# Optimization experiments

Measured on AMD Instinct MI355X. Metric: run time of the kernel, lower is better.

Reference implementation:

```python
import jax, jax.numpy as jnp
import numpy as np

HIDDEN = 1024
B, S = 4, 2048

def setup_inputs() -> dict:
    key = jax.random.key(0)
    k1, k2 = jax.random.split(key)
    qkv = jax.random.normal(k1, (B, S, HIDDEN), dtype=jnp.float32)
    mask = jnp.ones((B, S), dtype=jnp.float32)
    W_qkv = jax.random.normal(k2, (HIDDEN, 3 * HIDDEN), dtype=jnp.float32) * (HIDDEN ** -0.5)
    b_qkv = jnp.zeros((3 * HIDDEN,), dtype=jnp.float32)
    return {"qkv": qkv, "mask": mask, "W_qkv": W_qkv, "b_qkv": b_qkv}

def reference(qkv, mask, W_qkv, b_qkv):
    scale = HIDDEN ** -0.5
    proj = jnp.einsum("bsi,ih->bsh", qkv, W_qkv) + b_qkv  # [B,S,3H]
    q, k, v = jnp.split(proj, 3, axis=-1)                  # each [B,S,H]
    q = q * scale
    scores = jnp.einsum("bqh,bkh->bqk", q, k)              # [B,S,S]
    scores = scores + (1.0 - mask)[:, None, :] * -10000.0
    dist = jax.nn.softmax(scores, axis=-1)                 # dropout = identity (eval)
    return jnp.einsum("bqk,bkh->bqh", dist, v)             # [B,S,H]
```

## Files before the change

### kernel.cpp

```cpp
#include <hip/hip_runtime.h>
#include <hip/hip_bf16.h>

#define HID   1024
#define H3    3072
#define SEQ   2048
#define NB    4
#define MTOT  8192

typedef __bf16 bf16;
typedef bf16  bf16x4 __attribute__((ext_vector_type(4)));
typedef bf16  bf16x8 __attribute__((ext_vector_type(8)));
typedef float f32x4  __attribute__((ext_vector_type(4)));

#define MFMA16(a, b, c) __builtin_amdgcn_mfma_f32_16x16x32_bf16((a), (b), (c), 0, 0, 0)

#define GLOAD_LDS16(gp, lp)                                                     \
    __builtin_amdgcn_global_load_lds(                                           \
        (const __attribute__((address_space(1))) void*)(gp),                    \
        (__attribute__((address_space(3))) void*)(lp), 16, 0, 0)

#define FENCE() asm volatile("" ::: "memory")

__device__ __forceinline__ void stage_half(
    const bf16* __restrict__ G, long ld, long row0, long col0,
    char* dstbase, int w, int lane)
{
    const int r  = lane >> 2;
    const int c0 = ((lane & 3) * 8) ^ (((lane >> 5) & 1) << 4);
#pragma unroll
    for (int l = 0; l < 2; ++l) {
        const int sh = l * 8 + w;
        const bf16* src = G + (row0 + (long)((sh >> 1) * 16 + r)) * ld
                            + col0 + ((sh & 1) * 32 + c0);
        GLOAD_LDS16(src, dstbase + sh * 1024);
    }
}

__device__ __forceinline__ void gemm256_core(
    const bf16* __restrict__ A, long lda,
    const bf16* __restrict__ Bt, long ldb,
    long m0, long n0, int NT, char* lds, f32x4 (&acc)[8][4])
{
    const int tid = threadIdx.x, lane = tid & 63, w = tid >> 6;
    const int lr = lane & 15, lkg = lane >> 4;
    const int subA = (w >> 2) * 8;
    const int subB = (w & 3) * 4;
    const int inner = lr * 64 + (((lkg * 8) ^ ((lr >> 3) << 4)) << 1);

    char* A0b = lds;
    char* B0b = lds + 32768;
    char* A1b = lds + 65536;
    char* B1b = lds + 98304;

    stage_half(A,  lda, m0,        0, A0b,          w, lane);
    stage_half(A,  lda, m0 + 128,  0, A0b + 16384,  w, lane);
    stage_half(Bt, ldb, n0,        0, B0b,          w, lane);
    stage_half(Bt, ldb, n0 + 128,  0, B0b + 16384,  w, lane);
    stage_half(Bt, ldb, n0,       64, B1b,          w, lane);
    stage_half(Bt, ldb, n0 + 128, 64, B1b + 16384,  w, lane);
    asm volatile("s_waitcnt vmcnt(0)" ::: "memory");
    __builtin_amdgcn_s_barrier();
    FENCE();

    bf16x8 aR[4][2], bR[4][2];

    for (int t = 0; t < NT; ++t) {
        char* Ac = (t & 1) ? A1b : A0b;
        char* Bc = (t & 1) ? B1b : B0b;
        char* An = (t & 1) ? A0b : A1b;
        const long kA = (long)(t + 1) * 64;
        const long kB = (long)(t + 2) * 64;
        const bool doA = (t + 1 < NT), doB = (t + 2 < NT);

#pragma unroll
        for (int mf = 0; mf < 4; ++mf)
#pragma unroll
            for (int ks = 0; ks < 2; ++ks)
                aR[mf][ks] = *(const bf16x8*)(Ac + ((subA + mf) * 2 + ks) * 1024 + inner);
#pragma unroll
        for (int nf = 0; nf < 2; ++nf)
#pragma unroll
            for (int ks = 0; ks < 2; ++ks)
                bR[nf][ks] = *(const bf16x8*)(Bc + ((subB + nf) * 2 + ks) * 1024 + inner);
        if (doA) stage_half(A, lda, m0, kA, An, w, lane);
        __builtin_amdgcn_s_barrier();
        __builtin_amdgcn_s_setprio(1);
#pragma unroll
        for (int mf = 0; mf < 4; ++mf)
#pragma unroll
            for (int nf = 0; nf < 2; ++nf)
#pragma unroll
                for (int ks = 0; ks < 2; ++ks)
                    acc[mf][nf] = MFMA16(aR[mf][ks], bR[nf][ks], acc[mf][nf]);
        __builtin_amdgcn_s_setprio(0);
        __builtin_amdgcn_s_barrier();
        FENCE();

#pragma unroll
        for (int nf = 0; nf < 2; ++nf)
#pragma unroll
            for (int ks = 0; ks < 2; ++ks)
                bR[2 + nf][ks] = *(const bf16x8*)(Bc + ((subB + 2 + nf) * 2 + ks) * 1024 + inner);
        if (doA) stage_half(A, lda, m0 + 128, kA, An + 16384, w, lane);
        __builtin_amdgcn_s_barrier();
        __builtin_amdgcn_s_setprio(1);
#pragma unroll
        for (int mf = 0; mf < 4; ++mf)
#pragma unroll
            for (int nf = 0; nf < 2; ++nf)
#pragma unroll
                for (int ks = 0; ks < 2; ++ks)
                    acc[mf][2 + nf] = MFMA16(aR[mf][ks], bR[2 + nf][ks], acc[mf][2 + nf]);
        __builtin_amdgcn_s_setprio(0);
        __builtin_amdgcn_s_barrier();
        FENCE();

#pragma unroll
        for (int mf = 0; mf < 4; ++mf)
#pragma unroll
            for (int ks = 0; ks < 2; ++ks)
                aR[mf][ks] = *(const bf16x8*)(Ac + ((subA + 4 + mf) * 2 + ks) * 1024 + inner);
        if (doB) stage_half(Bt, ldb, n0, kB, Bc, w, lane);
        __builtin_amdgcn_s_barrier();
        __builtin_amdgcn_s_setprio(1);
#pragma unroll
        for (int mf = 0; mf < 4; ++mf)
#pragma unroll
            for (int nf = 0; nf < 2; ++nf)
#pragma unroll
                for (int ks = 0; ks < 2; ++ks)
                    acc[4 + mf][nf] = MFMA16(aR[mf][ks], bR[nf][ks], acc[4 + mf][nf]);
        __builtin_amdgcn_s_setprio(0);
        __builtin_amdgcn_s_barrier();
        FENCE();

        if (doB) {
            stage_half(Bt, ldb, n0 + 128, kB, Bc + 16384, w, lane);
            asm volatile("s_waitcnt vmcnt(4)" ::: "memory");
        } else {
            asm volatile("s_waitcnt vmcnt(0)" ::: "memory");
        }
        __builtin_amdgcn_s_barrier();
        __builtin_amdgcn_s_setprio(1);
#pragma unroll
        for (int mf = 0; mf < 4; ++mf)
#pragma unroll
            for (int nf = 0; nf < 2; ++nf)
#pragma unroll
                for (int ks = 0; ks < 2; ++ks)
                    acc[4 + mf][2 + nf] = MFMA16(aR[mf][ks], bR[2 + nf][ks], acc[4 + mf][2 + nf]);
        __builtin_amdgcn_s_setprio(0);
        __builtin_amdgcn_s_barrier();
        FENCE();
    }
}

__device__ __forceinline__ void gemm_h_core(
    const bf16* __restrict__ A, long lda,
    const bf16* __restrict__ Bt, long ldb,
    long m0, long n0, int NT, char* lds, f32x4 (&acc)[4][4])
{
    const int tid = threadIdx.x, lane = tid & 63, w = tid >> 6;
    const int lr = lane & 15, lkg = lane >> 4;
    const int subA = (w >> 2) * 4;
    const int subB = (w & 3) * 4;
    const int inner = lr * 64 + (((lkg * 8) ^ ((lr >> 3) << 4)) << 1);

    char* A0b = lds;
    char* B0b = lds + 16384;
    char* A1b = lds + 49152;
    char* B1b = lds + 65536;

    stage_half(A,  lda, m0,        0, A0b,          w, lane);
    stage_half(Bt, ldb, n0,        0, B0b,          w, lane);
    stage_half(Bt, ldb, n0 + 128,  0, B0b + 16384,  w, lane);
    stage_half(Bt, ldb, n0,       64, B1b,          w, lane);
    stage_half(Bt, ldb, n0 + 128, 64, B1b + 16384,  w, lane);
    asm volatile("s_waitcnt vmcnt(0)" ::: "memory");
    __builtin_amdgcn_s_barrier();
    FENCE();

    bf16x8 aR[2][2], bR[4][2];

    for (int t = 0; t < NT; ++t) {
        char* Ac = (t & 1) ? A1b : A0b;
        char* Bc = (t & 1) ? B1b : B0b;
        char* An = (t & 1) ? A0b : A1b;
        const long kA = (long)(t + 1) * 64;
        const long kB = (long)(t + 2) * 64;
        const bool doA = (t + 1 < NT), doB = (t + 2 < NT);

#pragma unroll
        for (int mf = 0; mf < 2; ++mf)
#pragma unroll
            for (int ks = 0; ks < 2; ++ks)
                aR[mf][ks] = *(const bf16x8*)(Ac + ((subA + mf) * 2 + ks) * 1024 + inner);
#pragma unroll
        for (int nf = 0; nf < 2; ++nf)
#pragma unroll
            for (int ks = 0; ks < 2; ++ks)
                bR[nf][ks] = *(const bf16x8*)(Bc + ((subB + nf) * 2 + ks) * 1024 + inner);
        if (doA) stage_half(A, lda, m0, kA, An, w, lane);
        __builtin_amdgcn_s_barrier();
        __builtin_amdgcn_s_setprio(1);
#pragma unroll
        for (int mf = 0; mf < 2; ++mf)
#pragma unroll
            for (int nf = 0; nf < 2; ++nf)
#pragma unroll
                for (int ks = 0; ks < 2; ++ks)
                    acc[mf][nf] = MFMA16(aR[mf][ks], bR[nf][ks], acc[mf][nf]);
        __builtin_amdgcn_s_setprio(0);
        __builtin_amdgcn_s_barrier();
        FENCE();

#pragma unroll
        for (int nf = 0; nf < 2; ++nf)
#pragma unroll
            for (int ks = 0; ks < 2; ++ks)
                bR[2 + nf][ks] = *(const bf16x8*)(Bc + ((subB + 2 + nf) * 2 + ks) * 1024 + inner);
        __builtin_amdgcn_s_barrier();
        __builtin_amdgcn_s_setprio(1);
#pragma unroll
        for (int mf = 0; mf < 2; ++mf)
#pragma unroll
            for (int nf = 0; nf < 2; ++nf)
#pragma unroll
                for (int ks = 0; ks < 2; ++ks)
                    acc[mf][2 + nf] = MFMA16(aR[mf][ks], bR[2 + nf][ks], acc[mf][2 + nf]);
        __builtin_amdgcn_s_setprio(0);
        __builtin_amdgcn_s_barrier();
        FENCE();

#pragma unroll
        for (int mf = 0; mf < 2; ++mf)
#pragma unroll
            for (int ks = 0; ks < 2; ++ks)
                aR[mf][ks] = *(const bf16x8*)(Ac + ((subA + 2 + mf) * 2 + ks) * 1024 + inner);
        if (doB) {
            stage_half(Bt, ldb, n0,       kB, Bc,         w, lane);
            stage_half(Bt, ldb, n0 + 128, kB, Bc + 16384, w, lane);
        }
        __builtin_amdgcn_s_barrier();
        __builtin_amdgcn_s_setprio(1);
#pragma unroll
        for (int mf = 0; mf < 2; ++mf)
#pragma unroll
            for (int nf = 0; nf < 2; ++nf)
#pragma unroll
                for (int ks = 0; ks < 2; ++ks)
                    acc[2 + mf][nf] = MFMA16(aR[mf][ks], bR[nf][ks], acc[2 + mf][nf]);
        __builtin_amdgcn_s_setprio(0);
        __builtin_amdgcn_s_barrier();
        FENCE();

        if (doB) {
            asm volatile("s_waitcnt vmcnt(4)" ::: "memory");
        } else {
            asm volatile("s_waitcnt vmcnt(0)" ::: "memory");
        }
        __builtin_amdgcn_s_barrier();
        __builtin_amdgcn_s_setprio(1);
#pragma unroll
        for (int mf = 0; mf < 2; ++mf)
#pragma unroll
            for (int nf = 0; nf < 2; ++nf)
#pragma unroll
                for (int ks = 0; ks < 2; ++ks)
                    acc[2 + mf][2 + nf] = MFMA16(aR[mf][ks], bR[2 + nf][ks], acc[2 + mf][2 + nf]);
        __builtin_amdgcn_s_setprio(0);
        __builtin_amdgcn_s_barrier();
        FENCE();
    }
}

__global__ __launch_bounds__(256) void conv_kernel(
    const float* __restrict__ X, const float* __restrict__ W,
    bf16* __restrict__ Xb, bf16* __restrict__ Wt, float* __restrict__ lbuf)
{
    __shared__ bf16 T[64][66];
    const int bid = blockIdx.x;
    if (bid < 4096) {
        const long i = ((long)bid * 256 + threadIdx.x) * 8;
        float4 a = *(const float4*)(X + i);
        float4 b = *(const float4*)(X + i + 4);
        bf16x8 o;
        o[0] = (bf16)a.x; o[1] = (bf16)a.y; o[2] = (bf16)a.z; o[3] = (bf16)a.w;
        o[4] = (bf16)b.x; o[5] = (bf16)b.y; o[6] = (bf16)b.z; o[7] = (bf16)b.w;
        *(bf16x8*)(Xb + i) = o;
    } else if (bid < 4096 + 768) {
        const int b2 = bid - 4096;
        const int n0 = (b2 % 48) * 64, k0 = (b2 / 48) * 64;
        const int r = threadIdx.x >> 2, s = threadIdx.x & 3;
        const float* wp = W + (size_t)(k0 + r) * H3 + n0 + s * 16;
#pragma unroll
        for (int q = 0; q < 4; ++q) {
            float4 a = *(const float4*)(wp + q * 4);
            T[r][s * 16 + q * 4 + 0] = (bf16)a.x;
            T[r][s * 16 + q * 4 + 1] = (bf16)a.y;
            T[r][s * 16 + q * 4 + 2] = (bf16)a.z;
            T[r][s * 16 + q * 4 + 3] = (bf16)a.w;
        }
        __syncthreads();
        bf16x8 o0, o1;
#pragma unroll
        for (int i = 0; i < 8; ++i) o0[i] = T[s * 16 + i][r];
#pragma unroll
        for (int i = 0; i < 8; ++i) o1[i] = T[s * 16 + 8 + i][r];
        bf16* op = Wt + (size_t)(n0 + r) * HID + k0 + s * 16;
        *(bf16x8*)op       = o0;
        *(bf16x8*)(op + 8) = o1;
    } else {
        for (int i = threadIdx.x; i < MTOT; i += 256) lbuf[i] = 0.0f;
    }
}

__global__ __launch_bounds__(512, 2) void proj_h(
    const bf16* __restrict__ Xb, const bf16* __restrict__ Wt,
    const float* __restrict__ bias,
    bf16* __restrict__ Qb, bf16* __restrict__ Kb, bf16* __restrict__ Vt)
{
    __shared__ __attribute__((aligned(16))) char lds[98304];
    const int x = blockIdx.x & 7, q = blockIdx.x >> 3;
    const int bm = x * 8 + (q & 7);
    const int bn = q >> 3;

    f32x4 acc[4][4] = {};
    gemm_h_core(Xb, HID, Wt, HID, (long)bm * 128, (long)bn * 256, 16, lds, acc);

    const int tid = threadIdx.x, lane = tid & 63, w = tid >> 6;
    const int lr = lane & 15, lkg = lane >> 4;
    const int wmL = (w >> 2) * 64;
    const int wnL = (w & 3) * 64;
    const int seg = bn >> 2;

    __syncthreads();
    bf16* sm_ = (bf16*)lds;

    if (seg < 2) {
        const float qs = (seg == 0) ? 0.03125f : 1.0f;
#pragma unroll
        for (int nf = 0; nf < 4; ++nf) {
            const int nl = wnL + nf * 16 + lr;
            const float bv = bias[bn * 256 + nl];
#pragma unroll
            for (int mf = 0; mf < 4; ++mf) {
                const int ml = wmL + mf * 16 + lkg * 4;
#pragma unroll
                for (int j = 0; j < 4; ++j)
                    sm_[(ml + j) * 264 + nl] = (bf16)((acc[mf][nf][j] + bv) * qs);
            }
        }
        __syncthreads();
        bf16* dst = (seg == 0) ? Qb : Kb;
        const long rowbase = (long)bm * 128;
        const long colbase = (long)(bn & 3) * 256;
#pragma unroll
        for (int it = 0; it < 8; ++it) {
            const int ml = (tid >> 5) + it * 16;
            const int nc = (tid & 31) * 8;
            bf16x8 vv = *(const bf16x8*)&sm_[ml * 264 + nc];
            *(bf16x8*)&dst[(rowbase + ml) * HID + colbase + nc] = vv;
        }
    } else {
#pragma unroll
        for (int nf = 0; nf < 4; ++nf) {
            const int nl = wnL + nf * 16 + lr;
            const float bv = bias[bn * 256 + nl];
#pragma unroll
            for (int mf = 0; mf < 4; ++mf) {
                const int ml = wmL + mf * 16 + lkg * 4;
                bf16x4 pk;
#pragma unroll
                for (int j = 0; j < 4; ++j) pk[j] = (bf16)(acc[mf][nf][j] + bv);
                *(bf16x4*)&sm_[nl * 136 + ml] = pk;
            }
        }
        __syncthreads();
        const int  bb = bm >> 4;
        const long s0 = (long)(bm & 15) * 128;
        const long h0 = (long)(bn - 8) * 256;
#pragma unroll
        for (int it = 0; it < 8; ++it) {
            const int nl = (tid >> 4) + it * 32;
            const int mc = (tid & 15) * 8;
            bf16x8 vv = *(const bf16x8*)&sm_[nl * 136 + mc];
            *(bf16x8*)&Vt[((long)(bb << 10) + h0 + nl) * SEQ + s0 + mc] = vv;
        }
    }
}

__global__ __launch_bounds__(512, 2) void qk_gemm2(
    const bf16* __restrict__ Qb, const bf16* __restrict__ Kb,
    bf16* __restrict__ Pb, float* __restrict__ lbuf,
    const float* __restrict__ mask, int b_base)
{
    __shared__ __attribute__((aligned(16))) char lds[135168];
    __shared__ float lsum[2][128][4];
    const int z = blockIdx.z, b = b_base + z;

    f32x4 acc[8][4] = {};
    gemm256_core(Qb + (size_t)b * SEQ * HID, HID,
                 Kb + (size_t)b * SEQ * HID, HID,
                 (long)blockIdx.x * 256, (long)blockIdx.y * 256, 16, lds, acc);

    const int tid = threadIdx.x, lane = tid & 63, w = tid >> 6;
    const int lr = lane & 15, lkg = lane >> 4;
    const int mh = w >> 2;
    const int nw = w & 3;

    __syncthreads();
    bf16* smP = (bf16*)lds;

    float mterm[4];
#pragma unroll
    for (int nf = 0; nf < 4; ++nf) {
        const int col = (int)blockIdx.y * 256 + nw * 64 + nf * 16 + lr;
        mterm[nf] = (1.0f - mask[(size_t)b * SEQ + col]) * -10000.0f;
    }

#pragma unroll
    for (int mf = 0; mf < 8; ++mf) {
#pragma unroll
        for (int j = 0; j < 4; ++j) {
            const int rloc = mf * 16 + lkg * 4 + j;
            float rs = 0.0f;
#pragma unroll
            for (int nf = 0; nf < 4; ++nf) {
                const float e = __expf(acc[mf][nf][j] + mterm[nf]);
                smP[(mh * 128 + rloc) * 264 + nw * 64 + nf * 16 + lr] = (bf16)e;
                rs += e;
            }
            rs += __shfl_xor(rs, 1);
            rs += __shfl_xor(rs, 2);
            rs += __shfl_xor(rs, 4);
            rs += __shfl_xor(rs, 8);
            if (lr == 0) lsum[mh][rloc][nw] = rs;
        }
    }
    __syncthreads();

    bf16* P = Pb + (size_t)z * SEQ * SEQ;
    const long rowbase = (long)blockIdx.x * 256;
    const long colbase = (long)blockIdx.y * 256;
#pragma unroll
    for (int it = 0; it < 16; ++it) {
        const int ml = (tid >> 5) + it * 16;
        const int nc = (tid & 31) * 8;
        bf16x8 vv = *(const bf16x8*)&smP[ml * 264 + nc];
        *(bf16x8*)&P[(rowbase + ml) * SEQ + colbase + nc] = vv;
    }

    if (tid < 256) {
        const int half = tid >> 7, r128 = tid & 127;
        const float s4 = lsum[half][r128][0] + lsum[half][r128][1]
                       + lsum[half][r128][2] + lsum[half][r128][3];
        atomicAdd(&lbuf[(size_t)b * SEQ + rowbase + tid], s4);
    }
}

__global__ __launch_bounds__(512, 2) void pv_gemm2(
    const bf16* __restrict__ Pb, const bf16* __restrict__ Vt,
    const float* __restrict__ lbuf, float* __restrict__ out, int b_base)
{
    __shared__ __attribute__((aligned(16))) char lds[98304];
    const int z = blockIdx.z, b = b_base + z;

    f32x4 acc[4][4] = {};
    gemm_h_core(Pb + (size_t)z * SEQ * SEQ, SEQ,
                Vt + (size_t)b * HID * SEQ, SEQ,
                (long)blockIdx.x * 128, (long)blockIdx.y * 256, 32, lds, acc);

    const int tid = threadIdx.x, lane = tid & 63, w = tid >> 6;
    const int lr = lane & 15, lkg = lane >> 4;
    const int m0i = (int)blockIdx.x * 128 + (w >> 2) * 64;
    const int n0i = (int)blockIdx.y * 256 + (w & 3) * 64;
    float* C = out + (size_t)b * SEQ * HID;
#pragma unroll
    for (int mf = 0; mf < 4; ++mf)
#pragma unroll
        for (int j = 0; j < 4; ++j) {
            const int row = m0i + mf * 16 + lkg * 4 + j;
            const float inv = 1.0f / lbuf[(size_t)b * SEQ + row];
#pragma unroll
            for (int nf = 0; nf < 4; ++nf)
                C[(size_t)row * HID + n0i + nf * 16 + lr] = acc[mf][nf][j] * inv;
        }
}

extern "C" void kernel_launch(void* const* d_in, const int* in_sizes, int n_in,
                              void* d_out, int out_size, void* d_ws, size_t ws_size,
                              hipStream_t stream)
{
    const float* X    = (const float*)d_in[0];
    const float* mask = (const float*)d_in[1];
    const float* W    = (const float*)d_in[2];
    const float* bias = (const float*)d_in[3];
    float* out = (float*)d_out;

    char* ws = (char*)d_ws;
    const size_t MB = 1024 * 1024;
    bf16*  Qb   = (bf16*)ws;
    bf16*  Kb   = (bf16*)(ws + 16 * MB);
    bf16*  Vt   = (bf16*)(ws + 32 * MB);
    float* lbuf = (float*)(ws + 48 * MB);
    bf16*  Xb   = (bf16*)(ws + 49 * MB);
    bf16*  Wt   = (bf16*)(ws + 65 * MB);
    bf16*  Pb   = (bf16*)(ws + 49 * MB);

    int nbg;
    if      (ws_size >= 81 * MB) nbg = 4;
    else if (ws_size >= 65 * MB) nbg = 2;
    else                         nbg = 1;

    conv_kernel<<<4096 + 768 + 1, 256, 0, stream>>>(X, W, Xb, Wt, lbuf);
    proj_h<<<768, 512, 0, stream>>>(Xb, Wt, bias, Qb, Kb, Vt);

    for (int g = 0; g < NB / nbg; ++g) {
        const int b0 = g * nbg;
        qk_gemm2<<<dim3(8, 8, nbg), 512, 0, stream>>>(Qb, Kb, Pb, lbuf, mask, b0);
        pv_gemm2<<<dim3(16, 4, nbg), 512, 0, stream>>>(Pb, Vt, lbuf, out, b0);
    }
}
```

Before: 158.3 us.

## Triple-buffer B tiles and merge GEMM inner loop into two MFMA phases

Rewrites the shared GEMM core used by the projection and PV kernels. B tiles now rotate through three LDS buffers and are prefetched two steps ahead, alongside the A prefetch. All four A fragments load into registers at once, so each k-step needs two MFMA phases instead of four, with fewer barriers. LDS per block grows to 128 KB, which limits blocks per CU and leaves little room for other shared memory.

```diff
diff --git a/kernel.cpp b/kernel.cpp
--- a/kernel.cpp
+++ b/kernel.cpp
@@ -155,7 +155,7 @@
     }
 }
 
-__device__ __forceinline__ void gemm_h_core(
+__device__ __forceinline__ void gemm_h2_core(
     const bf16* __restrict__ A, long lda,
     const bf16* __restrict__ Bt, long ldb,
     long m0, long n0, int NT, char* lds, f32x4 (&acc)[4][4])
@@ -166,32 +166,31 @@
     const int subB = (w & 3) * 4;
     const int inner = lr * 64 + (((lkg * 8) ^ ((lr >> 3) << 4)) << 1);
 
-    char* A0b = lds;
-    char* B0b = lds + 16384;
-    char* A1b = lds + 49152;
-    char* B1b = lds + 65536;
-
-    stage_half(A,  lda, m0,        0, A0b,          w, lane);
-    stage_half(Bt, ldb, n0,        0, B0b,          w, lane);
-    stage_half(Bt, ldb, n0 + 128,  0, B0b + 16384,  w, lane);
-    stage_half(Bt, ldb, n0,       64, B1b,          w, lane);
-    stage_half(Bt, ldb, n0 + 128, 64, B1b + 16384,  w, lane);
-    asm volatile("s_waitcnt vmcnt(0)" ::: "memory");
+    char* Ab[2] = { lds, lds + 16384 };
+    char* Bb[3] = { lds + 32768, lds + 65536, lds + 98304 };
+
+    stage_half(A,  lda, m0,        0, Ab[0],          w, lane);
+    stage_half(Bt, ldb, n0,        0, Bb[0],          w, lane);
+    stage_half(Bt, ldb, n0 + 128,  0, Bb[0] + 16384,  w, lane);
+    stage_half(Bt, ldb, n0,       64, Bb[1],          w, lane);
+    stage_half(Bt, ldb, n0 + 128, 64, Bb[1] + 16384,  w, lane);
+    asm volatile("s_waitcnt vmcnt(4)" ::: "memory");
     __builtin_amdgcn_s_barrier();
     FENCE();
 
-    bf16x8 aR[2][2], bR[4][2];
+    bf16x8 aR[4][2], bR[2][2];
 
     for (int t = 0; t < NT; ++t) {
-        char* Ac = (t & 1) ? A1b : A0b;
-        char* Bc = (t & 1) ? B1b : B0b;
-        char* An = (t & 1) ? A0b : A1b;
+        char* Ac = Ab[t & 1];
+        char* An = Ab[(t + 1) & 1];
+        char* Bc = Bb[t % 3];
+        char* Bs = Bb[(t + 2) % 3];
         const long kA = (long)(t + 1) * 64;
         const long kB = (long)(t + 2) * 64;
         const bool doA = (t + 1 < NT), doB = (t + 2 < NT);
 
 #pragma unroll
-        for (int mf = 0; mf < 2; ++mf)
+        for (int mf = 0; mf < 4; ++mf)
 #pragma unroll
             for (int ks = 0; ks < 2; ++ks)
                 aR[mf][ks] = *(const bf16x8*)(Ac + ((subA + mf) * 2 + ks) * 1024 + inner);
@@ -201,10 +200,14 @@
             for (int ks = 0; ks < 2; ++ks)
                 bR[nf][ks] = *(const bf16x8*)(Bc + ((subB + nf) * 2 + ks) * 1024 + inner);
         if (doA) stage_half(A, lda, m0, kA, An, w, lane);
-        __builtin_amdgcn_s_barrier();
-        __builtin_amdgcn_s_setprio(1);
-#pragma unroll
-        for (int mf = 0; mf < 2; ++mf)
+        if (doB) {
+            stage_half(Bt, ldb, n0,       kB, Bs,         w, lane);
+            stage_half(Bt, ldb, n0 + 128, kB, Bs + 16384, w, lane);
+        }
+        __builtin_amdgcn_s_barrier();
+        __builtin_amdgcn_s_setprio(1);
+#pragma unroll
+        for (int mf = 0; mf < 4; ++mf)
 #pragma unroll
             for (int nf = 0; nf < 2; ++nf)
 #pragma unroll
@@ -218,57 +221,22 @@
         for (int nf = 0; nf < 2; ++nf)
 #pragma unroll
             for (int ks = 0; ks < 2; ++ks)
-                bR[2 + nf][ks] = *(const bf16x8*)(Bc + ((subB + 2 + nf) * 2 + ks) * 1024 + inner);
-        __builtin_amdgcn_s_barrier();
-        __builtin_amdgcn_s_setprio(1);
-#pragma unroll
-        for (int mf = 0; mf < 2; ++mf)
-#pragma unroll
-            for (int nf = 0; nf < 2; ++nf)
-#pragma unroll
-                for (int ks = 0; ks < 2; ++ks)
-                    acc[mf][2 + nf] = MFMA16(aR[mf][ks], bR[2 + nf][ks], acc[mf][2 + nf]);
-        __builtin_amdgcn_s_setprio(0);
-        __builtin_amdgcn_s_barrier();
-        FENCE();
-
-#pragma unroll
-        for (int mf = 0; mf < 2; ++mf)
-#pragma unroll
-            for (int ks = 0; ks < 2; ++ks)
-                aR[mf][ks] = *(const bf16x8*)(Ac + ((subA + 2 + mf) * 2 + ks) * 1024 + inner);
-        if (doB) {
-            stage_half(Bt, ldb, n0,       kB, Bc,         w, lane);
-            stage_half(Bt, ldb, n0 + 128, kB, Bc + 16384, w, lane);
-        }
-        __builtin_amdgcn_s_barrier();
-        __builtin_amdgcn_s_setprio(1);
-#pragma unroll
-        for (int mf = 0; mf < 2; ++mf)
-#pragma unroll
-            for (int nf = 0; nf < 2; ++nf)
-#pragma unroll
-                for (int ks = 0; ks < 2; ++ks)
-                    acc[2 + mf][nf] = MFMA16(aR[mf][ks], bR[nf][ks], acc[2 + mf][nf]);
-        __builtin_amdgcn_s_setprio(0);
-        __builtin_amdgcn_s_barrier();
-        FENCE();
-
+                bR[nf][ks] = *(const bf16x8*)(Bc + ((subB + 2 + nf) * 2 + ks) * 1024 + inner);
+        __builtin_amdgcn_s_barrier();
+        __builtin_amdgcn_s_setprio(1);
+#pragma unroll
+        for (int mf = 0; mf < 4; ++mf)
+#pragma unroll
+            for (int nf = 0; nf < 2; ++nf)
+#pragma unroll
+                for (int ks = 0; ks < 2; ++ks)
+                    acc[mf][2 + nf] = MFMA16(aR[mf][ks], bR[nf][ks], acc[mf][2 + nf]);
+        __builtin_amdgcn_s_setprio(0);
         if (doB) {
             asm volatile("s_waitcnt vmcnt(4)" ::: "memory");
         } else {
             asm volatile("s_waitcnt vmcnt(0)" ::: "memory");
         }
-        __builtin_amdgcn_s_barrier();
-        __builtin_amdgcn_s_setprio(1);
-#pragma unroll
-        for (int mf = 0; mf < 2; ++mf)
-#pragma unroll
-            for (int nf = 0; nf < 2; ++nf)
-#pragma unroll
-                for (int ks = 0; ks < 2; ++ks)
-                    acc[2 + mf][2 + nf] = MFMA16(aR[mf][ks], bR[2 + nf][ks], acc[2 + mf][2 + nf]);
-        __builtin_amdgcn_s_setprio(0);
         __builtin_amdgcn_s_barrier();
         FENCE();
     }
@@ -320,13 +288,13 @@
     const float* __restrict__ bias,
     bf16* __restrict__ Qb, bf16* __restrict__ Kb, bf16* __restrict__ Vt)
 {
-    __shared__ __attribute__((aligned(16))) char lds[98304];
+    __shared__ __attribute__((aligned(16))) char lds[131072];
     const int x = blockIdx.x & 7, q = blockIdx.x >> 3;
     const int bm = x * 8 + (q & 7);
     const int bn = q >> 3;
 
     f32x4 acc[4][4] = {};
-    gemm_h_core(Xb, HID, Wt, HID, (long)bm * 128, (long)bn * 256, 16, lds, acc);
+    gemm_h2_core(Xb, HID, Wt, HID, (long)bm * 128, (long)bn * 256, 16, lds, acc);
 
     const int tid = threadIdx.x, lane = tid & 63, w = tid >> 6;
     const int lr = lane & 15, lkg = lane >> 4;
@@ -463,13 +431,13 @@
     const bf16* __restrict__ Pb, const bf16* __restrict__ Vt,
     const float* __restrict__ lbuf, float* __restrict__ out, int b_base)
 {
-    __shared__ __attribute__((aligned(16))) char lds[98304];
+    __shared__ __attribute__((aligned(16))) char lds[131072];
     const int z = blockIdx.z, b = b_base + z;
 
     f32x4 acc[4][4] = {};
-    gemm_h_core(Pb + (size_t)z * SEQ * SEQ, SEQ,
-                Vt + (size_t)b * HID * SEQ, SEQ,
-                (long)blockIdx.x * 128, (long)blockIdx.y * 256, 32, lds, acc);
+    gemm_h2_core(Pb + (size_t)z * SEQ * SEQ, SEQ,
+                 Vt + (size_t)b * HID * SEQ, SEQ,
+                 (long)blockIdx.x * 128, (long)blockIdx.y * 256, 32, lds, acc);
 
     const int tid = threadIdx.x, lane = tid & 63, w = tid >> 6;
     const int lr = lane & 15, lkg = lane >> 4;
```

Measured after the change: 223.1 us. 1.41x slower.

## Use 256x256 tiles for Q/K projection and keep 128x256 tiles for V

Applied to the files above, without the earlier changes.

The single projection kernel now launches a mixed grid. The first 256 blocks compute the Q and K columns with a larger 256x256 tile (gemm256_core, 8x4 accumulator fragments per wave). The remaining 256 blocks compute the V columns with the old 128x256 tile and the transposed store. This raises arithmetic intensity and cuts redundant operand loads for two thirds of the projection, and drops the block count from 768 to 512. In exchange it uses more LDS (135 KB) and more accumulator registers per block, which may hurt occupancy, and the blocks within one launch now do unequal amounts of work.

```diff
diff --git a/kernel.cpp b/kernel.cpp
--- a/kernel.cpp
+++ b/kernel.cpp
@@ -315,36 +315,36 @@
     }
 }
 
-__global__ __launch_bounds__(512, 2) void proj_h(
+__global__ __launch_bounds__(512, 2) void proj_mixed(
     const bf16* __restrict__ Xb, const bf16* __restrict__ Wt,
     const float* __restrict__ bias,
     bf16* __restrict__ Qb, bf16* __restrict__ Kb, bf16* __restrict__ Vt)
 {
-    __shared__ __attribute__((aligned(16))) char lds[98304];
-    const int x = blockIdx.x & 7, q = blockIdx.x >> 3;
-    const int bm = x * 8 + (q & 7);
-    const int bn = q >> 3;
-
-    f32x4 acc[4][4] = {};
-    gemm_h_core(Xb, HID, Wt, HID, (long)bm * 128, (long)bn * 256, 16, lds, acc);
-
+    __shared__ __attribute__((aligned(16))) char lds[135168];
+    const int bid = blockIdx.x;
     const int tid = threadIdx.x, lane = tid & 63, w = tid >> 6;
     const int lr = lane & 15, lkg = lane >> 4;
-    const int wmL = (w >> 2) * 64;
-    const int wnL = (w & 3) * 64;
-    const int seg = bn >> 2;
-
-    __syncthreads();
-    bf16* sm_ = (bf16*)lds;
-
-    if (seg < 2) {
+
+    if (bid < 256) {
+        const int x = bid & 7, q = bid >> 3;
+        const int bm = x * 4 + (q & 3);
+        const int bn = q >> 2;
+        f32x4 acc[8][4] = {};
+        gemm256_core(Xb, HID, Wt, HID, (long)bm * 256, (long)bn * 256, 16, lds, acc);
+
+        const int wmL = (w >> 2) * 128;
+        const int wnL = (w & 3) * 64;
+        const int seg = bn >> 2;
+
+        __syncthreads();
+        bf16* sm_ = (bf16*)lds;
         const float qs = (seg == 0) ? 0.03125f : 1.0f;
 #pragma unroll
         for (int nf = 0; nf < 4; ++nf) {
             const int nl = wnL + nf * 16 + lr;
             const float bv = bias[bn * 256 + nl];
 #pragma unroll
-            for (int mf = 0; mf < 4; ++mf) {
+            for (int mf = 0; mf < 8; ++mf) {
                 const int ml = wmL + mf * 16 + lkg * 4;
 #pragma unroll
                 for (int j = 0; j < 4; ++j)
@@ -353,20 +353,33 @@
         }
         __syncthreads();
         bf16* dst = (seg == 0) ? Qb : Kb;
-        const long rowbase = (long)bm * 128;
+        const long rowbase = (long)bm * 256;
         const long colbase = (long)(bn & 3) * 256;
 #pragma unroll
-        for (int it = 0; it < 8; ++it) {
+        for (int it = 0; it < 16; ++it) {
             const int ml = (tid >> 5) + it * 16;
             const int nc = (tid & 31) * 8;
             bf16x8 vv = *(const bf16x8*)&sm_[ml * 264 + nc];
             *(bf16x8*)&dst[(rowbase + ml) * HID + colbase + nc] = vv;
         }
     } else {
+        const int b2 = bid - 256;
+        const int x = b2 & 7, q2 = b2 >> 3;
+        const int vm = x * 8 + (q2 & 7);
+        const int vn = q2 >> 3;
+        f32x4 acc[4][4] = {};
+        gemm_h_core(Xb, HID, Wt, HID, (long)vm * 128, 2048 + (long)vn * 256,
+                    16, lds, acc);
+
+        const int wmL = (w >> 2) * 64;
+        const int wnL = (w & 3) * 64;
+
+        __syncthreads();
+        bf16* sm_ = (bf16*)lds;
 #pragma unroll
         for (int nf = 0; nf < 4; ++nf) {
             const int nl = wnL + nf * 16 + lr;
-            const float bv = bias[bn * 256 + nl];
+            const float bv = bias[2048 + vn * 256 + nl];
 #pragma unroll
             for (int mf = 0; mf < 4; ++mf) {
                 const int ml = wmL + mf * 16 + lkg * 4;
@@ -377,9 +390,9 @@
             }
         }
         __syncthreads();
-        const int  bb = bm >> 4;
-        const long s0 = (long)(bm & 15) * 128;
-        const long h0 = (long)(bn - 8) * 256;
+        const int  bb = vm >> 4;
+        const long s0 = (long)(vm & 15) * 128;
+        const long h0 = (long)vn * 256;
 #pragma unroll
         for (int it = 0; it < 8; ++it) {
             const int nl = (tid >> 4) + it * 32;
@@ -514,7 +527,7 @@
     else                         nbg = 1;
 
     conv_kernel<<<4096 + 768 + 1, 256, 0, stream>>>(X, W, Xb, Wt, lbuf);
-    proj_h<<<768, 512, 0, stream>>>(Xb, Wt, bias, Qb, Kb, Vt);
+    proj_mixed<<<512, 512, 0, stream>>>(Xb, Wt, bias, Qb, Kb, Vt);
 
     for (int g = 0; g < NB / nbg; ++g) {
         const int b0 = g * nbg;
```

New measurement: 153.1 us (median of 2 runs). -3.3%, faster.
